# Optimization experiments

Hardware: AMD Instinct MI355X
Metric: run time of the kernel (lower is better)

Reference implementation:

```python
import jax, jax.numpy as jnp
import numpy as np

D_MODEL = 1024
N_HEADS = 16
D_K = D_MODEL // N_HEADS
CAUSAL = True


def setup_inputs() -> dict:
    key = jax.random.key(0)
    ks = jax.random.split(key, 11)
    B, S, D = 2, 2048, D_MODEL
    scale = 1.0 / np.sqrt(D)
    inp = {
        "in_Q": jax.random.normal(ks[0], (B, S, D), jnp.float32),
        "in_K": jax.random.normal(ks[1], (B, S, D), jnp.float32),
        "in_V": jax.random.normal(ks[2], (B, S, D), jnp.float32),
        # torch Linear params: weight [out, in], bias [out]
        "Wq": jax.random.normal(ks[3], (D, D), jnp.float32) * scale,
        "bq": jax.random.normal(ks[4], (D,), jnp.float32) * scale,
        "Wk": jax.random.normal(ks[5], (D, D), jnp.float32) * scale,
        "bk": jax.random.normal(ks[6], (D,), jnp.float32) * scale,
        "Wv": jax.random.normal(ks[7], (D, D), jnp.float32) * scale,
        "bv": jax.random.normal(ks[8], (D,), jnp.float32) * scale,
        "Wo": jax.random.normal(ks[9], (D, D), jnp.float32) * scale,
        "bo": jax.random.normal(ks[10], (D,), jnp.float32) * scale,
    }
    return inp


def reference(in_Q, in_K, in_V, Wq, bq, Wk, bk, Wv, bv, Wo, bo):
    B, S, D = in_Q.shape
    H, dk = N_HEADS, D_K
    # Linear projections (torch: x @ W.T + b)
    Q = in_Q @ Wq.T + bq
    K = in_K @ Wk.T + bk
    V = in_V @ Wv.T + bv
    # split heads: [B, S, D] -> [B, H, S, dk]
    Qh = Q.reshape(B, S, H, dk).transpose(0, 2, 1, 3)
    Kh = K.reshape(B, S, H, dk).transpose(0, 2, 1, 3)
    Vh = V.reshape(B, S, H, dk).transpose(0, 2, 1, 3)
    # scores [B, H, S, S]
    scores = jnp.einsum("bhqd,bhkd->bhqk", Qh, Kh) / jnp.sqrt(jnp.float32(dk))
    if CAUSAL:
        mask = jnp.tril(jnp.ones((S, S), dtype=bool))
        scores = jnp.where(mask, scores, -jnp.inf)
    attn = jax.nn.softmax(scores, axis=-1)
    out = jnp.einsum("bhqk,bhkd->bhqd", attn, Vh)
    Hcat = out.transpose(0, 2, 1, 3).reshape(B, S, D)
    return Hcat @ Wo.T + bo
```

## Files before the change

### kernel.cpp

```cpp
#include <hip/hip_runtime.h>
#include <hip/hip_bf16.h>
#include <math.h>

#define D_MODEL 1024
#define NHEADS  16
#define DK      64
#define SEQ     2048
#define BATCH   2
#define MROWS   4096
#define NQT     (SEQ/64)

typedef unsigned short ushort_t;
using short8 = __attribute__((ext_vector_type(8))) short;
using f32x4  = __attribute__((ext_vector_type(4))) float;

__device__ __forceinline__ ushort_t f2bf(float x) {
    unsigned u = __float_as_uint(x);
    u = (u + 0x7FFFu + ((u >> 16) & 1u)) >> 16;
    return (ushort_t)u;
}

__device__ __forceinline__ unsigned pk2(float a, float b) {
    __hip_bfloat162 h = __float22bfloat162_rn(float2{a, b});
    unsigned u;
    __builtin_memcpy(&u, &h, 4);
    return u;
}

__device__ __forceinline__ void gll16(const ushort_t* g, ushort_t* l) {
    __builtin_amdgcn_global_load_lds(
        (const __attribute__((address_space(1))) void*)(g),
        (__attribute__((address_space(3))) void*)(l), 16, 0, 0);
}

__global__ __launch_bounds__(256) void cvt_bf16(
    const float* s0, const float* s1, const float* s2, const float* s3,
    const float* s4, const float* s5, const float* s6,
    ushort_t* d0, ushort_t* d1, ushort_t* d2, ushort_t* d3,
    ushort_t* d4, ushort_t* d5, ushort_t* d6, int nIn, int nW)
{
    const float* s; ushort_t* d; int n;
    switch (blockIdx.y) {
        case 0: s = s0; d = d0; n = nIn; break;
        case 1: s = s1; d = d1; n = nIn; break;
        case 2: s = s2; d = d2; n = nIn; break;
        case 3: s = s3; d = d3; n = nW;  break;
        case 4: s = s4; d = d4; n = nW;  break;
        case 5: s = s5; d = d5; n = nW;  break;
        default: s = s6; d = d6; n = nW; break;
    }
    int i = (blockIdx.x * 256 + threadIdx.x) * 4;
    if (i < n) {
        float4 v = *(const float4*)&s[i];
        ushort4 o;
        o.x = f2bf(v.x); o.y = f2bf(v.y); o.z = f2bf(v.z); o.w = f2bf(v.w);
        *(ushort4*)&d[i] = o;
    }
}

struct GemmArgs { const ushort_t* A; const ushort_t* W; const float* bias;
                  void* C; int mode; float oscale; };

template<int MODE>
__device__ __forceinline__ void gemm_core(const GemmArgs& ga,
                                          ushort_t* As, ushort_t* Bs)
{
    const int tid  = threadIdx.x;
    const int w    = tid >> 6, lane = tid & 63;
    const int quad = lane >> 4, lx = lane & 15;
    const int mw = (w >> 1) * 64, nw = (w & 1) * 64;
    const int bm = (MODE == 1 ? blockIdx.y : blockIdx.x) * 128;
    const int bn = (MODE == 1 ? blockIdx.x : blockIdx.y) * 128;
    const int K = D_MODEL;

    f32x4 acc[4][4];
#pragma unroll
    for (int mt = 0; mt < 4; ++mt)
#pragma unroll
        for (int nt = 0; nt < 4; ++nt)
            acc[mt][nt] = (f32x4){0.f, 0.f, 0.f, 0.f};

    float4 b4[4];
    float  bfr[4];
#pragma unroll
    for (int i = 0; i < 4; ++i) {
        if (MODE == 0) b4[i]  = *(const float4*)&ga.bias[bn + nw + i * 16 + quad * 4];
        else           bfr[i] = ga.bias[bm + mw + i * 16 + lx];
    }

    for (int k0 = 0; k0 < K; k0 += 64) {
        __syncthreads();
#pragma unroll
        for (int i = 0; i < 4; ++i) {
            int r0 = (w * 4 + i) * 8;
            int rl = r0 + (lane >> 3);
            int g  = (lane & 7) ^ (rl & 7);
            gll16(&ga.A[(size_t)(bm + rl) * K + k0 + g * 8], &As[r0 * 64]);
            gll16(&ga.W[(size_t)(bn + rl) * K + k0 + g * 8], &Bs[r0 * 64]);
        }
        __syncthreads();

#pragma unroll
        for (int ks = 0; ks < 2; ++ks) {
            short8 af[4], bf[4];
#pragma unroll
            for (int mt = 0; mt < 4; ++mt) {
                int r = mw + mt * 16 + lx;
                af[mt] = *(const short8*)&As[r * 64 + (((ks * 4 + quad) ^ (r & 7)) << 3)];
            }
#pragma unroll
            for (int nt = 0; nt < 4; ++nt) {
                int r = nw + nt * 16 + lx;
                bf[nt] = *(const short8*)&Bs[r * 64 + (((ks * 4 + quad) ^ (r & 7)) << 3)];
            }
#pragma unroll
            for (int mt = 0; mt < 4; ++mt)
#pragma unroll
                for (int nt = 0; nt < 4; ++nt)
                    acc[mt][nt] = __builtin_amdgcn_mfma_f32_16x16x32_bf16(
                        bf[nt], af[mt], acc[mt][nt], 0, 0, 0);
        }
    }

    if (MODE == 0) {
        ushort_t* C = (ushort_t*)ga.C;
        const float os = ga.oscale;
#pragma unroll
        for (int mt = 0; mt < 4; ++mt) {
            int m = bm + mw + mt * 16 + lx;
#pragma unroll
            for (int nt = 0; nt < 4; ++nt) {
                int n0 = bn + nw + nt * 16 + quad * 4;
                uint2 u;
                u.x = pk2((acc[mt][nt][0] + b4[nt].x) * os, (acc[mt][nt][1] + b4[nt].y) * os);
                u.y = pk2((acc[mt][nt][2] + b4[nt].z) * os, (acc[mt][nt][3] + b4[nt].w) * os);
                *(uint2*)&C[(size_t)m * D_MODEL + n0] = u;
            }
        }
    } else {
        ushort_t* C = (ushort_t*)ga.C;
#pragma unroll
        for (int mt = 0; mt < 4; ++mt) {
            int ch = bm + mw + mt * 16 + lx;
            int h = ch >> 6, d = ch & 63;
            float bb = bfr[mt];
#pragma unroll
            for (int nt = 0; nt < 4; ++nt) {
                int n0 = bn + nw + nt * 16 + quad * 4;
                int b = n0 >> 11, s0 = n0 & 2047;
                uint2 u;
                u.x = pk2(acc[mt][nt][0] + bb, acc[mt][nt][1] + bb);
                u.y = pk2(acc[mt][nt][2] + bb, acc[mt][nt][3] + bb);
                *(uint2*)&C[((size_t)(b * NHEADS + h) * DK + d) * SEQ + s0] = u;
            }
        }
    }
}

__global__ __launch_bounds__(256) void gemm_mfma(GemmArgs g0, GemmArgs g1, GemmArgs g2)
{
    __shared__ ushort_t As[128 * 64];
    __shared__ ushort_t Bs[128 * 64];
    GemmArgs ga = (blockIdx.z == 0) ? g0 : ((blockIdx.z == 1) ? g1 : g2);
    if (ga.mode == 0) gemm_core<0>(ga, As, Bs);
    else              gemm_core<1>(ga, As, Bs);
}

__global__ __launch_bounds__(256) void gemm_o(
    const ushort_t* __restrict__ A, const ushort_t* __restrict__ W,
    const float* __restrict__ bias, float* __restrict__ C)
{
    __shared__ ushort_t As[64 * 64];
    __shared__ ushort_t Bs[128 * 64];

    const int tid  = threadIdx.x;
    const int w    = tid >> 6, lane = tid & 63;
    const int quad = lane >> 4, lx = lane & 15;
    const int mw = (w >> 1) * 32, nw = (w & 1) * 64;
    const int bm = blockIdx.x * 64, bn = blockIdx.y * 128;
    const int K = D_MODEL;

    f32x4 acc[2][4];
#pragma unroll
    for (int mt = 0; mt < 2; ++mt)
#pragma unroll
        for (int nt = 0; nt < 4; ++nt)
            acc[mt][nt] = (f32x4){0.f, 0.f, 0.f, 0.f};

    float4 b4[4];
#pragma unroll
    for (int nt = 0; nt < 4; ++nt)
        b4[nt] = *(const float4*)&bias[bn + nw + nt * 16 + quad * 4];

    for (int k0 = 0; k0 < K; k0 += 64) {
        __syncthreads();
#pragma unroll
        for (int i = 0; i < 2; ++i) {
            int r0 = (i * 4 + w) * 8;
            int rl = r0 + (lane >> 3);
            int g  = (lane & 7) ^ (rl & 7);
            gll16(&A[(size_t)(bm + rl) * K + k0 + g * 8], &As[r0 * 64]);
        }
#pragma unroll
        for (int i = 0; i < 4; ++i) {
            int r0 = (i * 4 + w) * 8;
            int rl = r0 + (lane >> 3);
            int g  = (lane & 7) ^ (rl & 7);
            gll16(&W[(size_t)(bn + rl) * K + k0 + g * 8], &Bs[r0 * 64]);
        }
        __syncthreads();

#pragma unroll
        for (int ks = 0; ks < 2; ++ks) {
            short8 af[2], bf[4];
#pragma unroll
            for (int mt = 0; mt < 2; ++mt) {
                int r = mw + mt * 16 + lx;
                af[mt] = *(const short8*)&As[r * 64 + (((ks * 4 + quad) ^ (r & 7)) << 3)];
            }
#pragma unroll
            for (int nt = 0; nt < 4; ++nt) {
                int r = nw + nt * 16 + lx;
                bf[nt] = *(const short8*)&Bs[r * 64 + (((ks * 4 + quad) ^ (r & 7)) << 3)];
            }
#pragma unroll
            for (int mt = 0; mt < 2; ++mt)
#pragma unroll
                for (int nt = 0; nt < 4; ++nt)
                    acc[mt][nt] = __builtin_amdgcn_mfma_f32_16x16x32_bf16(
                        bf[nt], af[mt], acc[mt][nt], 0, 0, 0);
        }
    }

#pragma unroll
    for (int mt = 0; mt < 2; ++mt) {
        int m = bm + mw + mt * 16 + lx;
#pragma unroll
        for (int nt = 0; nt < 4; ++nt) {
            int n0 = bn + nw + nt * 16 + quad * 4;
            float4 v;
            v.x = acc[mt][nt][0] + b4[nt].x;
            v.y = acc[mt][nt][1] + b4[nt].y;
            v.z = acc[mt][nt][2] + b4[nt].z;
            v.w = acc[mt][nt][3] + b4[nt].w;
            *(float4*)&C[(size_t)m * D_MODEL + n0] = v;
        }
    }
}

__device__ __forceinline__ void flash_tile(
    int qt, const size_t qbase, const size_t vbase,
    const ushort_t* __restrict__ Qp, const ushort_t* __restrict__ Kp,
    const ushort_t* __restrict__ Vt, ushort_t* __restrict__ Hc,
    ushort_t* Ks0, ushort_t* Ks1, ushort_t* Vs0, ushort_t* Vs1,
    ushort_t (*Ps)[16 * 64])
{
    const int tid  = threadIdx.x;
    const int w    = tid >> 6, lane = tid & 63;
    const int quad = lane >> 4, lx = lane & 15;

    {
#pragma unroll
        for (int i = 0; i < 2; ++i) {
            int r0 = (w + i * 4) * 8;
            int rl = r0 + (lane >> 3);
            int g  = (lane & 7) ^ (rl & 7);
            gll16(&Kp[qbase + (size_t)rl * D_MODEL + g * 8], &Ks0[r0 * 64]);
            gll16(&Vt[vbase + (size_t)rl * SEQ + g * 8], &Vs0[r0 * 64]);
        }
    }

    short8 qf[2];
    {
        size_t ro = qbase + (size_t)(qt * 64 + w * 16 + lx) * D_MODEL + quad * 8;
        qf[0] = *(const short8*)&Qp[ro];
        qf[1] = *(const short8*)&Qp[ro + 32];
    }

    char* Pb = (char*)&Ps[w][0] + (lx << 7);
    const int hsw = (lx & 7) << 4;

    f32x4 O[4];
#pragma unroll
    for (int nt = 0; nt < 4; ++nt) O[nt] = (f32x4){0.f, 0.f, 0.f, 0.f};
    float mrow = -INFINITY, lrow = 0.f;
    const int qin = w * 16 + lx;

    for (int kt = 0; kt <= qt; ++kt) {
        ushort_t* Ks = (kt & 1) ? Ks1 : Ks0;
        ushort_t* Vs = (kt & 1) ? Vs1 : Vs0;

        asm volatile("s_waitcnt vmcnt(0)" ::: "memory");
        asm volatile("s_barrier" ::: "memory");

        if (kt < qt) {
            ushort_t* Kn = (kt & 1) ? Ks0 : Ks1;
            ushort_t* Vn = (kt & 1) ? Vs0 : Vs1;
#pragma unroll
            for (int i = 0; i < 2; ++i) {
                int r0 = (w + i * 4) * 8;
                int rl = r0 + (lane >> 3);
                int g  = (lane & 7) ^ (rl & 7);
                gll16(&Kp[qbase + (size_t)((kt + 1) * 64 + rl) * D_MODEL + g * 8], &Kn[r0 * 64]);
                gll16(&Vt[vbase + (size_t)rl * SEQ + (kt + 1) * 64 + g * 8], &Vn[r0 * 64]);
            }
        }

        f32x4 s[4];
        __builtin_amdgcn_s_setprio(1);
#pragma unroll
        for (int nt = 0; nt < 4; ++nt) {
            int r = nt * 16 + lx;
            short8 kf0 = *(const short8*)&Ks[r * 64 + ((quad ^ (r & 7)) << 3)];
            short8 kf1 = *(const short8*)&Ks[r * 64 + (((4 + quad) ^ (r & 7)) << 3)];
            f32x4 z = (f32x4){0.f, 0.f, 0.f, 0.f};
            z = __builtin_amdgcn_mfma_f32_16x16x32_bf16(kf0, qf[0], z, 0, 0, 0);
            z = __builtin_amdgcn_mfma_f32_16x16x32_bf16(kf1, qf[1], z, 0, 0, 0);
            s[nt] = z;
        }
        __builtin_amdgcn_s_setprio(0);

        if (kt == qt) {
#pragma unroll
            for (int nt = 0; nt < 4; ++nt)
#pragma unroll
                for (int r = 0; r < 4; ++r)
                    if ((nt * 16 + quad * 4 + r) > qin) s[nt][r] = -INFINITY;
        }

        float a0 = fmaxf(fmaxf(s[0][0], s[0][1]), fmaxf(s[0][2], s[0][3]));
        float a1 = fmaxf(fmaxf(s[1][0], s[1][1]), fmaxf(s[1][2], s[1][3]));
        float a2 = fmaxf(fmaxf(s[2][0], s[2][1]), fmaxf(s[2][2], s[2][3]));
        float a3 = fmaxf(fmaxf(s[3][0], s[3][1]), fmaxf(s[3][2], s[3][3]));
        float lm = fmaxf(fmaxf(a0, a1), fmaxf(a2, a3));
        if (__any(lm > mrow + 8.f)) {
            float tm = fmaxf(lm, __shfl_xor(lm, 16, 64));
            tm = fmaxf(tm, __shfl_xor(tm, 32, 64));
            float mnew = fmaxf(mrow, tm);
            float alpha = __builtin_amdgcn_exp2f(mrow - mnew);
            mrow = mnew;
            lrow *= alpha;
#pragma unroll
            for (int nt = 0; nt < 4; ++nt)
#pragma unroll
                for (int r = 0; r < 4; ++r) O[nt][r] *= alpha;
        }
#pragma unroll
        for (int nt = 0; nt < 4; ++nt)
#pragma unroll
            for (int r = 0; r < 4; ++r)
                s[nt][r] = __builtin_amdgcn_exp2f(s[nt][r] - mrow);
        float r0s = (s[0][0] + s[0][1]) + (s[0][2] + s[0][3]);
        float r1s = (s[1][0] + s[1][1]) + (s[1][2] + s[1][3]);
        float r2s = (s[2][0] + s[2][1]) + (s[2][2] + s[2][3]);
        float r3s = (s[3][0] + s[3][1]) + (s[3][2] + s[3][3]);
        lrow += (r0s + r1s) + (r2s + r3s);

#pragma unroll
        for (int nt = 0; nt < 4; ++nt) {
            uint2 u;
            u.x = pk2(s[nt][0], s[nt][1]);
            u.y = pk2(s[nt][2], s[nt][3]);
            *(uint2*)(Pb + ((nt * 32 + quad * 8) ^ hsw)) = u;
        }

        short8 pf0 = *(const short8*)(Pb + ((quad * 16) ^ hsw));
        short8 pf1 = *(const short8*)(Pb + ((64 + quad * 16) ^ hsw));

        __builtin_amdgcn_s_setprio(1);
#pragma unroll
        for (int nt = 0; nt < 4; ++nt) {
            int r = nt * 16 + lx;
            short8 vf0 = *(const short8*)&Vs[r * 64 + ((quad ^ (r & 7)) << 3)];
            short8 vf1 = *(const short8*)&Vs[r * 64 + (((4 + quad) ^ (r & 7)) << 3)];
            O[nt] = __builtin_amdgcn_mfma_f32_16x16x32_bf16(vf0, pf0, O[nt], 0, 0, 0);
            O[nt] = __builtin_amdgcn_mfma_f32_16x16x32_bf16(vf1, pf1, O[nt], 0, 0, 0);
        }
        __builtin_amdgcn_s_setprio(0);
    }

    {
        lrow += __shfl_xor(lrow, 16, 64);
        lrow += __shfl_xor(lrow, 32, 64);
        float invl = 1.f / lrow;
        size_t ro = qbase + (size_t)(qt * 64 + w * 16 + lx) * D_MODEL;
#pragma unroll
        for (int nt = 0; nt < 4; ++nt) {
            uint2 u;
            u.x = pk2(O[nt][0] * invl, O[nt][1] * invl);
            u.y = pk2(O[nt][2] * invl, O[nt][3] * invl);
            *(uint2*)&Hc[ro + nt * 16 + quad * 4] = u;
        }
    }
}

__global__ __launch_bounds__(256) void flash_mfma(
    const ushort_t* __restrict__ Qp, const ushort_t* __restrict__ Kp,
    const ushort_t* __restrict__ Vt, ushort_t* __restrict__ Hc)
{
    __shared__ ushort_t Ks0[64 * 64], Ks1[64 * 64];
    __shared__ ushort_t Vs0[64 * 64], Vs1[64 * 64];
    __shared__ __align__(16) ushort_t Ps[4][16 * 64];

    const int flat = blockIdx.x;
    const int c  = flat & 7;
    const int j  = flat >> 3;
    const int cu = j & 31;
    const int m  = j >> 5;
    const int bh = c + (m << 3);
    const int u  = (cu + ((m >> 1) << 3)) & 31;
    const int qt = (m & 1) ? (NQT - 1 - u) : u;
    const int b = bh >> 4, h = bh & 15;

    const size_t qbase = (size_t)(b * SEQ) * D_MODEL + h * DK;
    const size_t vbase = (size_t)bh * DK * SEQ;

    flash_tile(qt, qbase, vbase, Qp, Kp, Vt, Hc, Ks0, Ks1, Vs0, Vs1, Ps);
}

extern "C" void kernel_launch(void* const* d_in, const int* in_sizes, int n_in,
                              void* d_out, int out_size, void* d_ws, size_t ws_size,
                              hipStream_t stream) {
    const float* inQ = (const float*)d_in[0];
    const float* inK = (const float*)d_in[1];
    const float* inV = (const float*)d_in[2];
    const float* Wq  = (const float*)d_in[3];
    const float* bq  = (const float*)d_in[4];
    const float* Wk  = (const float*)d_in[5];
    const float* bk  = (const float*)d_in[6];
    const float* Wv  = (const float*)d_in[7];
    const float* bv  = (const float*)d_in[8];
    const float* Wo  = (const float*)d_in[9];
    const float* bo  = (const float*)d_in[10];
    float* out = (float*)d_out;

    const size_t NI = (size_t)MROWS * D_MODEL;
    const size_t NW = (size_t)D_MODEL * D_MODEL;
    ushort_t* ws  = (ushort_t*)d_ws;
    ushort_t* Qb  = ws;
    ushort_t* Kb  = Qb  + NI;
    ushort_t* Vb  = Kb  + NI;
    ushort_t* Wqb = Vb  + NI;
    ushort_t* Wkb = Wqb + NW;
    ushort_t* Wvb = Wkb + NW;
    ushort_t* Wob = Wvb + NW;
    ushort_t* Qp  = Wob + NW;
    ushort_t* Kp  = Qp  + NI;
    ushort_t* Vtg = Kp  + NI;
    ushort_t* Hc  = Vtg + NI;

    cvt_bf16<<<dim3(NI / 1024, 7), 256, 0, stream>>>(
        inQ, inK, inV, Wq, Wk, Wv, Wo,
        Qb, Kb, Vb, Wqb, Wkb, Wvb, Wob, (int)NI, (int)NW);

    const float qsc = 0.125f * 1.44269504088896340736f;
    GemmArgs aq{Qb, Wqb, bq, (void*)Qp, 0, qsc};
    GemmArgs ak{Kb, Wkb, bk, (void*)Kp, 0, 1.0f};
    GemmArgs av{Wvb, Vb, bv, (void*)Vtg, 1, 1.0f};
    gemm_mfma<<<dim3(MROWS / 128, D_MODEL / 128, 3), 256, 0, stream>>>(aq, ak, av);

    flash_mfma<<<dim3(NQT * BATCH * NHEADS), 256, 0, stream>>>(Qp, Kp, Vtg, Hc);

    gemm_o<<<dim3(MROWS / 64, D_MODEL / 128), 256, 0, stream>>>(Hc, Wob, bo, out);
}
```

Measured before the change: 212.9 us.

## Restructure flash attention to single-wave blocks with register-resident K/V fragments

The flash kernel drops its 4-wave blocks with LDS double-buffered K/V tiles. Each block is now a single wavefront handling 32 query rows as two 16-row groups, loading K and V fragments straight from global memory into registers with a K prefetch ping-pong. The grid is reordered to launch the longest causal tiles first, and block-level barriers go away. In exchange there is more register pressure, no LDS sharing of K/V across waves, and more redundant global and L2 traffic, since each wave re-reads the full K/V stream.

```diff
diff --git a/kernel.cpp b/kernel.cpp
--- a/kernel.cpp
+++ b/kernel.cpp
@@ -8,7 +8,7 @@
 #define SEQ     2048
 #define BATCH   2
 #define MROWS   4096
-#define NQT     (SEQ/64)
+#define NT2     (SEQ/32)
 
 typedef unsigned short ushort_t;
 using short8 = __attribute__((ext_vector_type(8))) short;
@@ -248,174 +248,220 @@
     }
 }
 
-__device__ __forceinline__ void flash_tile(
-    int qt, const size_t qbase, const size_t vbase,
-    const ushort_t* __restrict__ Qp, const ushort_t* __restrict__ Kp,
-    const ushort_t* __restrict__ Vt, ushort_t* __restrict__ Hc,
-    ushort_t* Ks0, ushort_t* Ks1, ushort_t* Vs0, ushort_t* Vs1,
-    ushort_t (*Ps)[16 * 64])
-{
-    const int tid  = threadIdx.x;
-    const int w    = tid >> 6, lane = tid & 63;
-    const int quad = lane >> 4, lx = lane & 15;
-
-    {
-#pragma unroll
-        for (int i = 0; i < 2; ++i) {
-            int r0 = (w + i * 4) * 8;
-            int rl = r0 + (lane >> 3);
-            int g  = (lane & 7) ^ (rl & 7);
-            gll16(&Kp[qbase + (size_t)rl * D_MODEL + g * 8], &Ks0[r0 * 64]);
-            gll16(&Vt[vbase + (size_t)rl * SEQ + g * 8], &Vs0[r0 * 64]);
-        }
-    }
-
-    short8 qf[2];
-    {
-        size_t ro = qbase + (size_t)(qt * 64 + w * 16 + lx) * D_MODEL + quad * 8;
-        qf[0] = *(const short8*)&Qp[ro];
-        qf[1] = *(const short8*)&Qp[ro + 32];
-    }
-
-    char* Pb = (char*)&Ps[w][0] + (lx << 7);
-    const int hsw = (lx & 7) << 4;
-
-    f32x4 O[4];
-#pragma unroll
-    for (int nt = 0; nt < 4; ++nt) O[nt] = (f32x4){0.f, 0.f, 0.f, 0.f};
-    float mrow = -INFINITY, lrow = 0.f;
-    const int qin = w * 16 + lx;
-
-    for (int kt = 0; kt <= qt; ++kt) {
-        ushort_t* Ks = (kt & 1) ? Ks1 : Ks0;
-        ushort_t* Vs = (kt & 1) ? Vs1 : Vs0;
-
-        asm volatile("s_waitcnt vmcnt(0)" ::: "memory");
-        asm volatile("s_barrier" ::: "memory");
-
-        if (kt < qt) {
-            ushort_t* Kn = (kt & 1) ? Ks0 : Ks1;
-            ushort_t* Vn = (kt & 1) ? Vs0 : Vs1;
-#pragma unroll
-            for (int i = 0; i < 2; ++i) {
-                int r0 = (w + i * 4) * 8;
-                int rl = r0 + (lane >> 3);
-                int g  = (lane & 7) ^ (rl & 7);
-                gll16(&Kp[qbase + (size_t)((kt + 1) * 64 + rl) * D_MODEL + g * 8], &Kn[r0 * 64]);
-                gll16(&Vt[vbase + (size_t)rl * SEQ + (kt + 1) * 64 + g * 8], &Vn[r0 * 64]);
-            }
-        }
-
-        f32x4 s[4];
-        __builtin_amdgcn_s_setprio(1);
-#pragma unroll
-        for (int nt = 0; nt < 4; ++nt) {
-            int r = nt * 16 + lx;
-            short8 kf0 = *(const short8*)&Ks[r * 64 + ((quad ^ (r & 7)) << 3)];
-            short8 kf1 = *(const short8*)&Ks[r * 64 + (((4 + quad) ^ (r & 7)) << 3)];
-            f32x4 z = (f32x4){0.f, 0.f, 0.f, 0.f};
-            z = __builtin_amdgcn_mfma_f32_16x16x32_bf16(kf0, qf[0], z, 0, 0, 0);
-            z = __builtin_amdgcn_mfma_f32_16x16x32_bf16(kf1, qf[1], z, 0, 0, 0);
-            s[nt] = z;
-        }
-        __builtin_amdgcn_s_setprio(0);
-
-        if (kt == qt) {
-#pragma unroll
-            for (int nt = 0; nt < 4; ++nt)
-#pragma unroll
-                for (int r = 0; r < 4; ++r)
-                    if ((nt * 16 + quad * 4 + r) > qin) s[nt][r] = -INFINITY;
-        }
-
-        float a0 = fmaxf(fmaxf(s[0][0], s[0][1]), fmaxf(s[0][2], s[0][3]));
-        float a1 = fmaxf(fmaxf(s[1][0], s[1][1]), fmaxf(s[1][2], s[1][3]));
-        float a2 = fmaxf(fmaxf(s[2][0], s[2][1]), fmaxf(s[2][2], s[2][3]));
-        float a3 = fmaxf(fmaxf(s[3][0], s[3][1]), fmaxf(s[3][2], s[3][3]));
-        float lm = fmaxf(fmaxf(a0, a1), fmaxf(a2, a3));
-        if (__any(lm > mrow + 8.f)) {
-            float tm = fmaxf(lm, __shfl_xor(lm, 16, 64));
-            tm = fmaxf(tm, __shfl_xor(tm, 32, 64));
-            float mnew = fmaxf(mrow, tm);
-            float alpha = __builtin_amdgcn_exp2f(mrow - mnew);
-            mrow = mnew;
-            lrow *= alpha;
-#pragma unroll
-            for (int nt = 0; nt < 4; ++nt)
-#pragma unroll
-                for (int r = 0; r < 4; ++r) O[nt][r] *= alpha;
-        }
-#pragma unroll
-        for (int nt = 0; nt < 4; ++nt)
-#pragma unroll
-            for (int r = 0; r < 4; ++r)
-                s[nt][r] = __builtin_amdgcn_exp2f(s[nt][r] - mrow);
-        float r0s = (s[0][0] + s[0][1]) + (s[0][2] + s[0][3]);
-        float r1s = (s[1][0] + s[1][1]) + (s[1][2] + s[1][3]);
-        float r2s = (s[2][0] + s[2][1]) + (s[2][2] + s[2][3]);
-        float r3s = (s[3][0] + s[3][1]) + (s[3][2] + s[3][3]);
-        lrow += (r0s + r1s) + (r2s + r3s);
-
-#pragma unroll
-        for (int nt = 0; nt < 4; ++nt) {
-            uint2 u;
-            u.x = pk2(s[nt][0], s[nt][1]);
-            u.y = pk2(s[nt][2], s[nt][3]);
-            *(uint2*)(Pb + ((nt * 32 + quad * 8) ^ hsw)) = u;
-        }
-
-        short8 pf0 = *(const short8*)(Pb + ((quad * 16) ^ hsw));
-        short8 pf1 = *(const short8*)(Pb + ((64 + quad * 16) ^ hsw));
-
-        __builtin_amdgcn_s_setprio(1);
-#pragma unroll
-        for (int nt = 0; nt < 4; ++nt) {
-            int r = nt * 16 + lx;
-            short8 vf0 = *(const short8*)&Vs[r * 64 + ((quad ^ (r & 7)) << 3)];
-            short8 vf1 = *(const short8*)&Vs[r * 64 + (((4 + quad) ^ (r & 7)) << 3)];
-            O[nt] = __builtin_amdgcn_mfma_f32_16x16x32_bf16(vf0, pf0, O[nt], 0, 0, 0);
-            O[nt] = __builtin_amdgcn_mfma_f32_16x16x32_bf16(vf1, pf1, O[nt], 0, 0, 0);
-        }
-        __builtin_amdgcn_s_setprio(0);
-    }
-
-    {
-        lrow += __shfl_xor(lrow, 16, 64);
-        lrow += __shfl_xor(lrow, 32, 64);
-        float invl = 1.f / lrow;
-        size_t ro = qbase + (size_t)(qt * 64 + w * 16 + lx) * D_MODEL;
-#pragma unroll
-        for (int nt = 0; nt < 4; ++nt) {
-            uint2 u;
-            u.x = pk2(O[nt][0] * invl, O[nt][1] * invl);
-            u.y = pk2(O[nt][2] * invl, O[nt][3] * invl);
-            *(uint2*)&Hc[ro + nt * 16 + quad * 4] = u;
-        }
-    }
-}
-
-__global__ __launch_bounds__(256) void flash_mfma(
+#define FLASH_BODY(CUR, NXT)                                                  \
+{                                                                             \
+                  \
+    f32x4 s0[4], s1[4];                                                       \
+    __builtin_amdgcn_s_setprio(1);                                            \
+    _Pragma("unroll")                                                         \
+    for (int nt = 0; nt < 4; ++nt) {                                          \
+        f32x4 z = (f32x4){0.f, 0.f, 0.f, 0.f};                                \
+        z = __builtin_amdgcn_mfma_f32_16x16x32_bf16(CUR[nt][0], qf[0][0], z, 0, 0, 0); \
+        z = __builtin_amdgcn_mfma_f32_16x16x32_bf16(CUR[nt][1], qf[0][1], z, 0, 0, 0); \
+        s0[nt] = z;                                                           \
+        f32x4 y = (f32x4){0.f, 0.f, 0.f, 0.f};                                \
+        y = __builtin_amdgcn_mfma_f32_16x16x32_bf16(CUR[nt][0], qf[1][0], y, 0, 0, 0); \
+        y = __builtin_amdgcn_mfma_f32_16x16x32_bf16(CUR[nt][1], qf[1][1], y, 0, 0, 0); \
+        s1[nt] = y;                                                           \
+    }                                                                         \
+    __builtin_amdgcn_s_setprio(0);                                            \
+           \
+    _Pragma("unroll")                                                         \
+    for (int nt = 0; nt < 4; ++nt) {                                          \
+        size_t vr = vbase + (size_t)(nt * 16 + lx) * SEQ + kt * 64 + quad * 8;\
+        vf[nt][0] = *(const short8*)&Vt[vr];                                  \
+        vf[nt][1] = *(const short8*)&Vt[vr + 32];                             \
+    }                                                                         \
+    if (kt < ktl) {                                                           \
+        _Pragma("unroll")                                                     \
+        for (int nt = 0; nt < 4; ++nt) {                                      \
+            size_t kr = qbase + (size_t)((kt + 1) * 64 + nt * 16 + lx) * D_MODEL + quad * 8; \
+            NXT[nt][0] = *(const short8*)&Kp[kr];                             \
+            NXT[nt][1] = *(const short8*)&Kp[kr + 32];                        \
+        }                                                                     \
+    }                                                                         \
+                                          \
+    if (kt == ktl) {                                                          \
+        int qr0 = t2 * 32 + lx - ktl * 64;                                    \
+        _Pragma("unroll")                                                     \
+        for (int nt = 0; nt < 4; ++nt)                                        \
+            _Pragma("unroll")                                                 \
+            for (int r = 0; r < 4; ++r) {                                     \
+                int kk = nt * 16 + quad * 4 + r;                              \
+                if (kk > qr0)      s0[nt][r] = -INFINITY;                     \
+                if (kk > qr0 + 16) s1[nt][r] = -INFINITY;                     \
+            }                                                                 \
+    }                                                                         \
+            \
+    {                                                                         \
+        float a0 = fmaxf(fmaxf(s0[0][0], s0[0][1]), fmaxf(s0[0][2], s0[0][3])); \
+        float a1 = fmaxf(fmaxf(s0[1][0], s0[1][1]), fmaxf(s0[1][2], s0[1][3])); \
+        float a2 = fmaxf(fmaxf(s0[2][0], s0[2][1]), fmaxf(s0[2][2], s0[2][3])); \
+        float a3 = fmaxf(fmaxf(s0[3][0], s0[3][1]), fmaxf(s0[3][2], s0[3][3])); \
+        float lm = fmaxf(fmaxf(a0, a1), fmaxf(a2, a3));                       \
+        if (__any(lm > mg[0] + 8.f)) {                                        \
+            float tm = fmaxf(lm, __shfl_xor(lm, 16, 64));                     \
+            tm = fmaxf(tm, __shfl_xor(tm, 32, 64));                          \
+            float mnew = fmaxf(mg[0], tm);                                    \
+            float alpha = __builtin_amdgcn_exp2f(mg[0] - mnew);               \
+            mg[0] = mnew; lg[0] *= alpha;                                     \
+            _Pragma("unroll")                                                 \
+            for (int nt = 0; nt < 4; ++nt)                                    \
+                _Pragma("unroll")                                             \
+                for (int r = 0; r < 4; ++r) O[0][nt][r] *= alpha;             \
+        }                                                                     \
+        _Pragma("unroll")                                                     \
+        for (int nt = 0; nt < 4; ++nt)                                        \
+            _Pragma("unroll")                                                 \
+            for (int r = 0; r < 4; ++r)                                       \
+                s0[nt][r] = __builtin_amdgcn_exp2f(s0[nt][r] - mg[0]);        \
+        lg[0] += ((s0[0][0]+s0[0][1])+(s0[0][2]+s0[0][3]))                    \
+               + ((s0[1][0]+s0[1][1])+(s0[1][2]+s0[1][3]))                    \
+               + ((s0[2][0]+s0[2][1])+(s0[2][2]+s0[2][3]))                    \
+               + ((s0[3][0]+s0[3][1])+(s0[3][2]+s0[3][3]));                   \
+    }                                                                         \
+                                                 \
+    {                                                                         \
+        float a0 = fmaxf(fmaxf(s1[0][0], s1[0][1]), fmaxf(s1[0][2], s1[0][3])); \
+        float a1 = fmaxf(fmaxf(s1[1][0], s1[1][1]), fmaxf(s1[1][2], s1[1][3])); \
+        float a2 = fmaxf(fmaxf(s1[2][0], s1[2][1]), fmaxf(s1[2][2], s1[2][3])); \
+        float a3 = fmaxf(fmaxf(s1[3][0], s1[3][1]), fmaxf(s1[3][2], s1[3][3])); \
+        float lm = fmaxf(fmaxf(a0, a1), fmaxf(a2, a3));                       \
+        if (__any(lm > mg[1] + 8.f)) {                                        \
+            float tm = fmaxf(lm, __shfl_xor(lm, 16, 64));                     \
+            tm = fmaxf(tm, __shfl_xor(tm, 32, 64));                          \
+            float mnew = fmaxf(mg[1], tm);                                    \
+            float alpha = __builtin_amdgcn_exp2f(mg[1] - mnew);               \
+            mg[1] = mnew; lg[1] *= alpha;                                     \
+            _Pragma("unroll")                                                 \
+            for (int nt = 0; nt < 4; ++nt)                                    \
+                _Pragma("unroll")                                             \
+                for (int r = 0; r < 4; ++r) O[1][nt][r] *= alpha;             \
+        }                                                                     \
+        _Pragma("unroll")                                                     \
+        for (int nt = 0; nt < 4; ++nt)                                        \
+            _Pragma("unroll")                                                 \
+            for (int r = 0; r < 4; ++r)                                       \
+                s1[nt][r] = __builtin_amdgcn_exp2f(s1[nt][r] - mg[1]);        \
+        lg[1] += ((s1[0][0]+s1[0][1])+(s1[0][2]+s1[0][3]))                    \
+               + ((s1[1][0]+s1[1][1])+(s1[1][2]+s1[1][3]))                    \
+               + ((s1[2][0]+s1[2][1])+(s1[2][2]+s1[2][3]))                    \
+               + ((s1[3][0]+s1[3][1])+(s1[3][2]+s1[3][3]));                   \
+    }                                                                         \
+                   \
+    {                                                                         \
+        _Pragma("unroll")                                                     \
+        for (int nt = 0; nt < 4; ++nt) {                                      \
+            uint2 u;                                                          \
+            u.x = pk2(s0[nt][0], s0[nt][1]);                                  \
+            u.y = pk2(s0[nt][2], s0[nt][3]);                                  \
+            *(uint2*)(Pb + ((nt * 32 + quad * 8) ^ hsw)) = u;                 \
+        }                                                                     \
+        short8 pf0 = *(const short8*)(Pb + ((quad * 16) ^ hsw));              \
+        short8 pf1 = *(const short8*)(Pb + ((64 + quad * 16) ^ hsw));         \
+        __builtin_amdgcn_s_setprio(1);                                        \
+        _Pragma("unroll")                                                     \
+        for (int nt = 0; nt < 4; ++nt) {                                      \
+            O[0][nt] = __builtin_amdgcn_mfma_f32_16x16x32_bf16(vf[nt][0], pf0, O[0][nt], 0, 0, 0); \
+            O[0][nt] = __builtin_amdgcn_mfma_f32_16x16x32_bf16(vf[nt][1], pf1, O[0][nt], 0, 0, 0); \
+        }                                                                     \
+        __builtin_amdgcn_s_setprio(0);                                        \
+    }                                                                         \
+      \
+    {                                                                         \
+        _Pragma("unroll")                                                     \
+        for (int nt = 0; nt < 4; ++nt) {                                      \
+            uint2 u;                                                          \
+            u.x = pk2(s1[nt][0], s1[nt][1]);                                  \
+            u.y = pk2(s1[nt][2], s1[nt][3]);                                  \
+            *(uint2*)(Pb + ((nt * 32 + quad * 8) ^ hsw)) = u;                 \
+        }                                                                     \
+        short8 pf0 = *(const short8*)(Pb + ((quad * 16) ^ hsw));              \
+        short8 pf1 = *(const short8*)(Pb + ((64 + quad * 16) ^ hsw));         \
+        __builtin_amdgcn_s_setprio(1);                                        \
+        _Pragma("unroll")                                                     \
+        for (int nt = 0; nt < 4; ++nt) {                                      \
+            O[1][nt] = __builtin_amdgcn_mfma_f32_16x16x32_bf16(vf[nt][0], pf0, O[1][nt], 0, 0, 0); \
+            O[1][nt] = __builtin_amdgcn_mfma_f32_16x16x32_bf16(vf[nt][1], pf1, O[1][nt], 0, 0, 0); \
+        }                                                                     \
+        __builtin_amdgcn_s_setprio(0);                                        \
+    }                                                                         \
+}
+
+__global__ __launch_bounds__(64, 2) void flash_mfma(
     const ushort_t* __restrict__ Qp, const ushort_t* __restrict__ Kp,
     const ushort_t* __restrict__ Vt, ushort_t* __restrict__ Hc)
 {
-    __shared__ ushort_t Ks0[64 * 64], Ks1[64 * 64];
-    __shared__ ushort_t Vs0[64 * 64], Vs1[64 * 64];
-    __shared__ __align__(16) ushort_t Ps[4][16 * 64];
+    __shared__ __align__(16) ushort_t Ps[16 * 64];
 
     const int flat = blockIdx.x;
     const int c  = flat & 7;
-    const int j  = flat >> 3;
-    const int cu = j & 31;
-    const int m  = j >> 5;
-    const int bh = c + (m << 3);
-    const int u  = (cu + ((m >> 1) << 3)) & 31;
-    const int qt = (m & 1) ? (NQT - 1 - u) : u;
+    const int b2 = (flat >> 3) & 3;
+    const int sidx = flat >> 5;
+    const int bh = c + (b2 << 3);
+    const int t2 = NT2 - 1 - sidx;
     const int b = bh >> 4, h = bh & 15;
 
     const size_t qbase = (size_t)(b * SEQ) * D_MODEL + h * DK;
     const size_t vbase = (size_t)bh * DK * SEQ;
 
-    flash_tile(qt, qbase, vbase, Qp, Kp, Vt, Hc, Ks0, Ks1, Vs0, Vs1, Ps);
+    const int lane = threadIdx.x;
+    const int quad = lane >> 4, lx = lane & 15;
+    const int ktl = (t2 * 32 + 31) >> 6;
+
+    short8 qf[2][2];
+#pragma unroll
+    for (int g = 0; g < 2; ++g) {
+        size_t ro = qbase + (size_t)(t2 * 32 + g * 16 + lx) * D_MODEL + quad * 8;
+        qf[g][0] = *(const short8*)&Qp[ro];
+        qf[g][1] = *(const short8*)&Qp[ro + 32];
+    }
+
+    char* Pb = (char*)&Ps[0] + (lx << 7);
+    const int hsw = (lx & 7) << 4;
+
+    f32x4 O[2][4];
+#pragma unroll
+    for (int g = 0; g < 2; ++g)
+#pragma unroll
+        for (int nt = 0; nt < 4; ++nt)
+            O[g][nt] = (f32x4){0.f, 0.f, 0.f, 0.f};
+    float mg[2] = {-INFINITY, -INFINITY};
+    float lg[2] = {0.f, 0.f};
+
+    short8 kfA[4][2], kfB[4][2], vf[4][2];
+#pragma unroll
+    for (int nt = 0; nt < 4; ++nt) {
+        size_t kr = qbase + (size_t)(nt * 16 + lx) * D_MODEL + quad * 8;
+        kfA[nt][0] = *(const short8*)&Kp[kr];
+        kfA[nt][1] = *(const short8*)&Kp[kr + 32];
+    }
+
+    int kt = 0;
+    for (;;) {
+        FLASH_BODY(kfA, kfB);
+        if (kt == ktl) break;
+        ++kt;
+        FLASH_BODY(kfB, kfA);
+        if (kt == ktl) break;
+        ++kt;
+    }
+
+#pragma unroll
+    for (int g = 0; g < 2; ++g) {
+        float l = lg[g];
+        l += __shfl_xor(l, 16, 64);
+        l += __shfl_xor(l, 32, 64);
+        float invl = 1.f / l;
+        size_t ro = qbase + (size_t)(t2 * 32 + g * 16 + lx) * D_MODEL;
+#pragma unroll
+        for (int nt = 0; nt < 4; ++nt) {
+            uint2 u;
+            u.x = pk2(O[g][nt][0] * invl, O[g][nt][1] * invl);
+            u.y = pk2(O[g][nt][2] * invl, O[g][nt][3] * invl);
+            *(uint2*)&Hc[ro + nt * 16 + quad * 4] = u;
+        }
+    }
 }
 
 extern "C" void kernel_launch(void* const* d_in, const int* in_sizes, int n_in,
@@ -459,7 +505,7 @@
     GemmArgs av{Wvb, Vb, bv, (void*)Vtg, 1, 1.0f};
     gemm_mfma<<<dim3(MROWS / 128, D_MODEL / 128, 3), 256, 0, stream>>>(aq, ak, av);
 
-    flash_mfma<<<dim3(NQT * BATCH * NHEADS), 256, 0, stream>>>(Qp, Kp, Vtg, Hc);
+    flash_mfma<<<dim3(NT2 * BATCH * NHEADS), 64, 0, stream>>>(Qp, Kp, Vtg, Hc);
 
     gemm_o<<<dim3(MROWS / 64, D_MODEL / 128), 256, 0, stream>>>(Hc, Wob, bo, out);
 }
```

Result: slower. 241.3 us (+13.4%).

## Fuse fp32-to-bf16 activation conversion into QKV projection GEMM loads

Applied to the files above, without the earlier changes.

Removes the separate bf16 conversion of the Q/K/V activation inputs and instead loads fp32 activations directly in the projection GEMM, converting to bf16 in registers before storing to swizzled LDS. Weights are still pre-converted by a smaller conversion kernel. This cuts a large intermediate write and reread of activations, but doubles per-tile global bytes for the activation operand and replaces asynchronous global-to-LDS loads with synchronous register loads.

```diff
diff --git a/kernel.cpp b/kernel.cpp
--- a/kernel.cpp
+++ b/kernel.cpp
@@ -35,30 +35,23 @@
 
 __global__ __launch_bounds__(256) void cvt_bf16(
     const float* s0, const float* s1, const float* s2, const float* s3,
-    const float* s4, const float* s5, const float* s6,
-    ushort_t* d0, ushort_t* d1, ushort_t* d2, ushort_t* d3,
-    ushort_t* d4, ushort_t* d5, ushort_t* d6, int nIn, int nW)
-{
-    const float* s; ushort_t* d; int n;
+    ushort_t* d0, ushort_t* d1, ushort_t* d2, ushort_t* d3)
+{
+    const float* s; ushort_t* d;
     switch (blockIdx.y) {
-        case 0: s = s0; d = d0; n = nIn; break;
-        case 1: s = s1; d = d1; n = nIn; break;
-        case 2: s = s2; d = d2; n = nIn; break;
-        case 3: s = s3; d = d3; n = nW;  break;
-        case 4: s = s4; d = d4; n = nW;  break;
-        case 5: s = s5; d = d5; n = nW;  break;
-        default: s = s6; d = d6; n = nW; break;
+        case 0: s = s0; d = d0; break;
+        case 1: s = s1; d = d1; break;
+        case 2: s = s2; d = d2; break;
+        default: s = s3; d = d3; break;
     }
     int i = (blockIdx.x * 256 + threadIdx.x) * 4;
-    if (i < n) {
-        float4 v = *(const float4*)&s[i];
-        ushort4 o;
-        o.x = f2bf(v.x); o.y = f2bf(v.y); o.z = f2bf(v.z); o.w = f2bf(v.w);
-        *(ushort4*)&d[i] = o;
-    }
-}
-
-struct GemmArgs { const ushort_t* A; const ushort_t* W; const float* bias;
+    float4 v = *(const float4*)&s[i];
+    ushort4 o;
+    o.x = f2bf(v.x); o.y = f2bf(v.y); o.z = f2bf(v.z); o.w = f2bf(v.w);
+    *(ushort4*)&d[i] = o;
+}
+
+struct GemmArgs { const float* X; const ushort_t* Wb; const float* bias;
                   void* C; int mode; float oscale; };
 
 template<int MODE>
@@ -73,6 +66,11 @@
     const int bn = (MODE == 1 ? blockIdx.x : blockIdx.y) * 128;
     const int K = D_MODEL;
 
+    ushort_t* Xs = (MODE == 0) ? As : Bs;
+    ushort_t* Ws = (MODE == 0) ? Bs : As;
+    const int xrow0 = (MODE == 0) ? bm : bn;
+    const int wrow0 = (MODE == 0) ? bn : bm;
+
     f32x4 acc[4][4];
 #pragma unroll
     for (int mt = 0; mt < 4; ++mt)
@@ -95,8 +93,19 @@
             int r0 = (w * 4 + i) * 8;
             int rl = r0 + (lane >> 3);
             int g  = (lane & 7) ^ (rl & 7);
-            gll16(&ga.A[(size_t)(bm + rl) * K + k0 + g * 8], &As[r0 * 64]);
-            gll16(&ga.W[(size_t)(bn + rl) * K + k0 + g * 8], &Bs[r0 * 64]);
+            gll16(&ga.Wb[(size_t)(wrow0 + rl) * K + k0 + g * 8], &Ws[r0 * 64]);
+        }
+#pragma unroll
+        for (int i = 0; i < 4; ++i) {
+            int r0 = (w * 4 + i) * 8;
+            int rl = r0 + (lane >> 3);
+            int cb = lane & 7;
+            const float4* p = (const float4*)&ga.X[(size_t)(xrow0 + rl) * K + k0 + cb * 8];
+            float4 v0 = p[0], v1 = p[1];
+            uint4 uu;
+            uu.x = pk2(v0.x, v0.y); uu.y = pk2(v0.z, v0.w);
+            uu.z = pk2(v1.x, v1.y); uu.w = pk2(v1.z, v1.w);
+            *(uint4*)&Xs[rl * 64 + ((cb ^ (rl & 7)) * 8)] = uu;
         }
         __syncthreads();
 
@@ -437,10 +446,7 @@
     const size_t NI = (size_t)MROWS * D_MODEL;
     const size_t NW = (size_t)D_MODEL * D_MODEL;
     ushort_t* ws  = (ushort_t*)d_ws;
-    ushort_t* Qb  = ws;
-    ushort_t* Kb  = Qb  + NI;
-    ushort_t* Vb  = Kb  + NI;
-    ushort_t* Wqb = Vb  + NI;
+    ushort_t* Wqb = ws;
     ushort_t* Wkb = Wqb + NW;
     ushort_t* Wvb = Wkb + NW;
     ushort_t* Wob = Wvb + NW;
@@ -449,14 +455,13 @@
     ushort_t* Vtg = Kp  + NI;
     ushort_t* Hc  = Vtg + NI;
 
-    cvt_bf16<<<dim3(NI / 1024, 7), 256, 0, stream>>>(
-        inQ, inK, inV, Wq, Wk, Wv, Wo,
-        Qb, Kb, Vb, Wqb, Wkb, Wvb, Wob, (int)NI, (int)NW);
+    cvt_bf16<<<dim3(NW / 1024, 4), 256, 0, stream>>>(
+        Wq, Wk, Wv, Wo, Wqb, Wkb, Wvb, Wob);
 
     const float qsc = 0.125f * 1.44269504088896340736f;
-    GemmArgs aq{Qb, Wqb, bq, (void*)Qp, 0, qsc};
-    GemmArgs ak{Kb, Wkb, bk, (void*)Kp, 0, 1.0f};
-    GemmArgs av{Wvb, Vb, bv, (void*)Vtg, 1, 1.0f};
+    GemmArgs aq{inQ, Wqb, bq, (void*)Qp, 0, qsc};
+    GemmArgs ak{inK, Wkb, bk, (void*)Kp, 0, 1.0f};
+    GemmArgs av{inV, Wvb, bv, (void*)Vtg, 1, 1.0f};
     gemm_mfma<<<dim3(MROWS / 128, D_MODEL / 128, 3), 256, 0, stream>>>(aq, ak, av);
 
     flash_mfma<<<dim3(NQT * BATCH * NHEADS), 256, 0, stream>>>(Qp, Kp, Vtg, Hc);
```

New measurement: 223.6 us. 1.05x slower.

## Remap GEMM blocks for XCD-aware L2 locality and double-buffer output projection

Applied to the files above, without the earlier changes.

The QKV GEMM launch now uses a flat 1D grid. The flat index is remapped so that blocks landing on the same chiplet (flat&7) share A-row tiles, which is meant to improve L2 reuse. The output projection kernel moves from 64x128 to 128x128 tiles with double-buffered LDS and prefetches the next k-tile during the MFMA loop, using raw waitcnt and barrier. This halves that kernel's grid to 256 blocks and raises LDS and register use, so occupancy falls and fewer blocks may not fill all CUs.

```diff
diff --git a/kernel.cpp b/kernel.cpp
--- a/kernel.cpp
+++ b/kernel.cpp
@@ -62,15 +62,15 @@
                   void* C; int mode; float oscale; };
 
 template<int MODE>
-__device__ __forceinline__ void gemm_core(const GemmArgs& ga,
+__device__ __forceinline__ void gemm_core(const GemmArgs& ga, int t32, int t8,
                                           ushort_t* As, ushort_t* Bs)
 {
     const int tid  = threadIdx.x;
     const int w    = tid >> 6, lane = tid & 63;
     const int quad = lane >> 4, lx = lane & 15;
     const int mw = (w >> 1) * 64, nw = (w & 1) * 64;
-    const int bm = (MODE == 1 ? blockIdx.y : blockIdx.x) * 128;
-    const int bn = (MODE == 1 ? blockIdx.x : blockIdx.y) * 128;
+    const int bm = (MODE == 1 ? t8 : t32) * 128;
+    const int bn = (MODE == 1 ? t32 : t8) * 128;
     const int K = D_MODEL;
 
     f32x4 acc[4][4];
@@ -161,28 +161,39 @@
 {
     __shared__ ushort_t As[128 * 64];
     __shared__ ushort_t Bs[128 * 64];
-    GemmArgs ga = (blockIdx.z == 0) ? g0 : ((blockIdx.z == 1) ? g1 : g2);
-    if (ga.mode == 0) gemm_core<0>(ga, As, Bs);
-    else              gemm_core<1>(ga, As, Bs);
+    const int flat = blockIdx.x;
+    const int c  = flat & 7;
+    const int rr = flat >> 3;
+    const int t32 = c * 4 + (rr & 3);
+    const int t8  = (rr >> 2) & 7;
+    const int z   = rr >> 5;
+    GemmArgs ga = (z == 0) ? g0 : ((z == 1) ? g1 : g2);
+    if (ga.mode == 0) gemm_core<0>(ga, t32, t8, As, Bs);
+    else              gemm_core<1>(ga, t32, t8, As, Bs);
 }
 
 __global__ __launch_bounds__(256) void gemm_o(
     const ushort_t* __restrict__ A, const ushort_t* __restrict__ W,
     const float* __restrict__ bias, float* __restrict__ C)
 {
-    __shared__ ushort_t As[64 * 64];
-    __shared__ ushort_t Bs[128 * 64];
+    __shared__ ushort_t As0[128 * 64], Bs0[128 * 64];
+    __shared__ ushort_t As1[128 * 64], Bs1[128 * 64];
+
+    const int flat = blockIdx.x;
+    const int c  = flat & 7;
+    const int rr = flat >> 3;
+    const int bm = (c * 4 + (rr & 3)) * 128;
+    const int bn = (rr >> 2) * 128;
 
     const int tid  = threadIdx.x;
     const int w    = tid >> 6, lane = tid & 63;
     const int quad = lane >> 4, lx = lane & 15;
-    const int mw = (w >> 1) * 32, nw = (w & 1) * 64;
-    const int bm = blockIdx.x * 64, bn = blockIdx.y * 128;
+    const int mw = (w >> 1) * 64, nw = (w & 1) * 64;
     const int K = D_MODEL;
 
-    f32x4 acc[2][4];
-#pragma unroll
-    for (int mt = 0; mt < 2; ++mt)
+    f32x4 acc[4][4];
+#pragma unroll
+    for (int mt = 0; mt < 4; ++mt)
 #pragma unroll
         for (int nt = 0; nt < 4; ++nt)
             acc[mt][nt] = (f32x4){0.f, 0.f, 0.f, 0.f};
@@ -192,39 +203,51 @@
     for (int nt = 0; nt < 4; ++nt)
         b4[nt] = *(const float4*)&bias[bn + nw + nt * 16 + quad * 4];
 
-    for (int k0 = 0; k0 < K; k0 += 64) {
-        __syncthreads();
-#pragma unroll
-        for (int i = 0; i < 2; ++i) {
-            int r0 = (i * 4 + w) * 8;
-            int rl = r0 + (lane >> 3);
-            int g  = (lane & 7) ^ (rl & 7);
-            gll16(&A[(size_t)(bm + rl) * K + k0 + g * 8], &As[r0 * 64]);
-        }
-#pragma unroll
-        for (int i = 0; i < 4; ++i) {
-            int r0 = (i * 4 + w) * 8;
-            int rl = r0 + (lane >> 3);
-            int g  = (lane & 7) ^ (rl & 7);
-            gll16(&W[(size_t)(bn + rl) * K + k0 + g * 8], &Bs[r0 * 64]);
-        }
-        __syncthreads();
+#pragma unroll
+    for (int i = 0; i < 4; ++i) {
+        int r0 = (w * 4 + i) * 8;
+        int rl = r0 + (lane >> 3);
+        int g  = (lane & 7) ^ (rl & 7);
+        gll16(&A[(size_t)(bm + rl) * K + g * 8], &As0[r0 * 64]);
+        gll16(&W[(size_t)(bn + rl) * K + g * 8], &Bs0[r0 * 64]);
+    }
+
+    for (int kt = 0; kt < 16; ++kt) {
+        ushort_t* Asr = (kt & 1) ? As1 : As0;
+        ushort_t* Bsr = (kt & 1) ? Bs1 : Bs0;
+
+        asm volatile("s_waitcnt vmcnt(0)" ::: "memory");
+        asm volatile("s_barrier" ::: "memory");
+
+        if (kt < 15) {
+            ushort_t* Asn = (kt & 1) ? As0 : As1;
+            ushort_t* Bsn = (kt & 1) ? Bs0 : Bs1;
+            int k0 = (kt + 1) * 64;
+#pragma unroll
+            for (int i = 0; i < 4; ++i) {
+                int r0 = (w * 4 + i) * 8;
+                int rl = r0 + (lane >> 3);
+                int g  = (lane & 7) ^ (rl & 7);
+                gll16(&A[(size_t)(bm + rl) * K + k0 + g * 8], &Asn[r0 * 64]);
+                gll16(&W[(size_t)(bn + rl) * K + k0 + g * 8], &Bsn[r0 * 64]);
+            }
+        }
 
 #pragma unroll
         for (int ks = 0; ks < 2; ++ks) {
-            short8 af[2], bf[4];
-#pragma unroll
-            for (int mt = 0; mt < 2; ++mt) {
+            short8 af[4], bf[4];
+#pragma unroll
+            for (int mt = 0; mt < 4; ++mt) {
                 int r = mw + mt * 16 + lx;
-                af[mt] = *(const short8*)&As[r * 64 + (((ks * 4 + quad) ^ (r & 7)) << 3)];
+                af[mt] = *(const short8*)&Asr[r * 64 + (((ks * 4 + quad) ^ (r & 7)) << 3)];
             }
 #pragma unroll
             for (int nt = 0; nt < 4; ++nt) {
                 int r = nw + nt * 16 + lx;
-                bf[nt] = *(const short8*)&Bs[r * 64 + (((ks * 4 + quad) ^ (r & 7)) << 3)];
-            }
-#pragma unroll
-            for (int mt = 0; mt < 2; ++mt)
+                bf[nt] = *(const short8*)&Bsr[r * 64 + (((ks * 4 + quad) ^ (r & 7)) << 3)];
+            }
+#pragma unroll
+            for (int mt = 0; mt < 4; ++mt)
 #pragma unroll
                 for (int nt = 0; nt < 4; ++nt)
                     acc[mt][nt] = __builtin_amdgcn_mfma_f32_16x16x32_bf16(
@@ -233,7 +256,7 @@
     }
 
 #pragma unroll
-    for (int mt = 0; mt < 2; ++mt) {
+    for (int mt = 0; mt < 4; ++mt) {
         int m = bm + mw + mt * 16 + lx;
 #pragma unroll
         for (int nt = 0; nt < 4; ++nt) {
@@ -457,9 +480,9 @@
     GemmArgs aq{Qb, Wqb, bq, (void*)Qp, 0, qsc};
     GemmArgs ak{Kb, Wkb, bk, (void*)Kp, 0, 1.0f};
     GemmArgs av{Wvb, Vb, bv, (void*)Vtg, 1, 1.0f};
-    gemm_mfma<<<dim3(MROWS / 128, D_MODEL / 128, 3), 256, 0, stream>>>(aq, ak, av);
+    gemm_mfma<<<dim3(768), 256, 0, stream>>>(aq, ak, av);
 
     flash_mfma<<<dim3(NQT * BATCH * NHEADS), 256, 0, stream>>>(Qp, Kp, Vtg, Hc);
 
-    gemm_o<<<dim3(MROWS / 64, D_MODEL / 128), 256, 0, stream>>>(Hc, Wob, bo, out);
-}
+    gemm_o<<<dim3(256), 256, 0, stream>>>(Hc, Wob, bo, out);
+}
```

Measured after the change: 224.4 us. +5.4%, slower.
